# Optimization experiments

Hardware: AMD Instinct MI355X
Metric: run time of the kernel (lower is better)

Reference implementation:

```python
import jax, jax.numpy as jnp
import numpy as np

N = 8192
F_IN = 512
F_HID = 256
ALPHA = 0.2  # LeakyReLU negative slope
NEG_INF = -9e15


def gat_layer(h, adj, W, a):
    """Standard dense GraphAttentionLayer (pyGAT style).
    h: [N, F_in], adj: [N, N] (0/1), W: [F_in, F_out], a: [2*F_out, 1].
    """
    Wh = h @ W  # [N, F_out]
    f_out = W.shape[1]
    # e_ij = leakyrelu(a1 . Wh_i + a2 . Wh_j) via broadcasting
    e1 = Wh @ a[:f_out]      # [N, 1]
    e2 = Wh @ a[f_out:]      # [N, 1]
    e = jax.nn.leaky_relu(e1 + e2.T, negative_slope=ALPHA)  # [N, N]
    e = jnp.where(adj > 0, e, NEG_INF)
    att = jax.nn.softmax(e, axis=-1)  # masked row softmax
    return jax.nn.elu(att @ Wh)       # [N, F_out]


def setup_inputs() -> dict:
    key = jax.random.key(0)
    k_x, k_adj, k_w1, k_a1, k_w2, k_a2 = jax.random.split(key, 6)
    x = jax.random.normal(k_x, (N, F_IN), dtype=jnp.float32)
    # sparse random adjacency (~avg degree 16) + self loops
    adj = (jax.random.uniform(k_adj, (N, N)) < (16.0 / N)).astype(jnp.float32)
    adj = jnp.clip(adj + jnp.eye(N, dtype=jnp.float32), 0.0, 1.0)
    # Xavier-ish init for layer params
    W1 = jax.random.normal(k_w1, (F_IN, F_HID), dtype=jnp.float32) * (1.0 / np.sqrt(F_IN))
    a1 = jax.random.normal(k_a1, (2 * F_HID, 1), dtype=jnp.float32) * (1.0 / np.sqrt(2 * F_HID))
    W2 = jax.random.normal(k_w2, (F_HID, F_IN), dtype=jnp.float32) * (1.0 / np.sqrt(F_HID))
    a2 = jax.random.normal(k_a2, (2 * F_IN, 1), dtype=jnp.float32) * (1.0 / np.sqrt(2 * F_IN))
    return {"x": x, "adj": adj, "W1": W1, "a1": a1, "W2": W2, "a2": a2}


def reference(x, adj, W1, a1, W2, a2):
    enc = gat_layer(x, adj, W1, a1)    # encode: [N, F_HID]
    dec = gat_layer(enc, adj, W2, a2)  # decode: [N, F_IN]
    return (dec, enc)
```

## Files before the change

kernel.cpp:

```cpp
#include <hip/hip_runtime.h>
#include <hip/hip_bf16.h>

#define N_NODES 8192
#define F_IN    512
#define F_HID   256
#define ALPHA   0.2f
#define MAXDEG  64

using f32x4 = __attribute__((ext_vector_type(4))) float;
using f16x8 = __attribute__((ext_vector_type(8))) _Float16;
using f16x4 = __attribute__((ext_vector_type(4))) _Float16;

__global__ void conv_WT(const float* __restrict__ W1, const float* __restrict__ W2,
                        _Float16* __restrict__ W1T, _Float16* __restrict__ W2T,
                        float* __restrict__ stz) {
    int gid = blockIdx.x * blockDim.x + threadIdx.x;
    if (gid < 4 * N_NODES) stz[gid] = 0.0f;

    int t = blockIdx.x;
    const float* W; _Float16* WT; int K, N, kt, nt;
    if (t < 128) { W = W1; WT = W1T; K = 512; N = 256; kt = t & 15; nt = t >> 4; }
    else { t -= 128; W = W2; WT = W2T; K = 256; N = 512; kt = t & 7; nt = t >> 3; }
    __shared__ float Ws[32][33];
    const int tx = threadIdx.x & 31, ty = threadIdx.x >> 5;
    #pragma unroll
    for (int i = 0; i < 4; ++i)
        Ws[ty + 8 * i][tx] = W[(size_t)(kt * 32 + ty + 8 * i) * N + nt * 32 + tx];
    __syncthreads();
    #pragma unroll
    for (int i = 0; i < 4; ++i)
        WT[(size_t)(nt * 32 + ty + 8 * i) * K + kt * 32 + tx] = (_Float16)Ws[tx][ty + 8 * i];
}

__device__ inline void csr_row(const float* __restrict__ adj, int* __restrict__ cols,
                               int* __restrict__ cnt, int row, int lane) {
    const float4* arow = (const float4*)(adj + (size_t)row * N_NODES);
    int* crow = cols + (size_t)row * MAXDEG;
    int count = 0;
    const unsigned long long mlt = (1ULL << lane) - 1ULL;
    for (int base = 0; base < N_NODES; base += 256) {
        float4 v = arow[(base >> 2) + lane];
        unsigned long long b0 = __ballot(v.x > 0.0f);
        unsigned long long b1 = __ballot(v.y > 0.0f);
        unsigned long long b2 = __ballot(v.z > 0.0f);
        unsigned long long b3 = __ballot(v.w > 0.0f);
        int o = count + __popcll(b0 & mlt) + __popcll(b1 & mlt)
                      + __popcll(b2 & mlt) + __popcll(b3 & mlt);
        int c0 = base + (lane << 2);
        if (v.x > 0.0f) { if (o < MAXDEG) crow[o] = c0;     o++; }
        if (v.y > 0.0f) { if (o < MAXDEG) crow[o] = c0 + 1; o++; }
        if (v.z > 0.0f) { if (o < MAXDEG) crow[o] = c0 + 2; o++; }
        if (v.w > 0.0f) { if (o < MAXDEG) crow[o] = c0 + 3; o++; }
        count += __popcll(b0) + __popcll(b1) + __popcll(b2) + __popcll(b3);
    }
    if (lane == 0) cnt[row] = count > MAXDEG ? MAXDEG : count;
}

__device__ inline void gemm1_tile(const float* __restrict__ x,
                                  const _Float16* __restrict__ W1T,
                                  _Float16* __restrict__ Wh1,
                                  const float* __restrict__ a1,
                                  float* __restrict__ s1, float* __restrict__ t1,
                                  int brow, int bcol) {
    const int LDT = 72;
    __shared__ _Float16 As[64 * LDT];
    __shared__ _Float16 Bs[64 * LDT];
    const int tid = threadIdx.x;
    const int wid = tid >> 6, lane = tid & 63;
    const int wr = (wid >> 1) * 32, wc = (wid & 1) * 32;
    const int sr = tid >> 3, skg = (tid & 7) * 8;

    f32x4 acc[2][2];
    #pragma unroll
    for (int m = 0; m < 2; ++m)
        #pragma unroll
        for (int n = 0; n < 2; ++n) acc[m][n] = f32x4{0.f, 0.f, 0.f, 0.f};

    for (int k0 = 0; k0 < F_IN; k0 += 64) {
        #pragma unroll
        for (int i = 0; i < 2; ++i) {
            int r = sr + i * 32;
            const float* src = x + (size_t)(brow + r) * F_IN + k0 + skg;
            f32x4 a0 = *(const f32x4*)src;
            f32x4 a1v = *(const f32x4*)(src + 4);
            f16x8 av;
            #pragma unroll
            for (int j = 0; j < 4; ++j) { av[j] = (_Float16)a0[j]; av[4 + j] = (_Float16)a1v[j]; }
            *(f16x8*)&As[r * LDT + skg] = av;
            *(f16x8*)&Bs[r * LDT + skg] = *(const f16x8*)&W1T[(size_t)(bcol + r) * F_IN + k0 + skg];
        }
        __syncthreads();
        #pragma unroll
        for (int ks = 0; ks < 2; ++ks) {
            const int kb = ks * 32 + (lane >> 4) * 8;
            f16x8 af[2], bfr[2];
            #pragma unroll
            for (int m = 0; m < 2; ++m)
                af[m] = *(const f16x8*)&As[(wr + m * 16 + (lane & 15)) * LDT + kb];
            #pragma unroll
            for (int n = 0; n < 2; ++n)
                bfr[n] = *(const f16x8*)&Bs[(wc + n * 16 + (lane & 15)) * LDT + kb];
            #pragma unroll
            for (int m = 0; m < 2; ++m)
                #pragma unroll
                for (int n = 0; n < 2; ++n)
                    acc[m][n] = __builtin_amdgcn_mfma_f32_16x16x32_f16(
                        af[m], bfr[n], acc[m][n], 0, 0, 0);
        }
        __syncthreads();
    }
    const int c0 = bcol + wc + (lane & 15);
    float as0 = a1[c0],      as1 = a1[c0 + 16];
    float at0 = a1[F_HID + c0], at1 = a1[F_HID + c0 + 16];
    #pragma unroll
    for (int m = 0; m < 2; ++m) {
        #pragma unroll
        for (int j = 0; j < 4; ++j) {
            float vs = acc[m][0][j] * as0 + acc[m][1][j] * as1;
            float vt = acc[m][0][j] * at0 + acc[m][1][j] * at1;
            #pragma unroll
            for (int off = 1; off < 16; off <<= 1) {
                vs += __shfl_xor(vs, off);
                vt += __shfl_xor(vt, off);
            }
            if ((lane & 15) == 0) {
                int row = brow + wr + m * 16 + ((lane >> 4) << 2) + j;
                atomicAdd(s1 + row, vs);
                atomicAdd(t1 + row, vt);
            }
        }
        #pragma unroll
        for (int n = 0; n < 2; ++n) {
            int row = brow + wr + m * 16 + ((lane >> 4) << 2);
            int col = bcol + wc + n * 16 + (lane & 15);
            #pragma unroll
            for (int j = 0; j < 4; ++j)
                Wh1[(size_t)(row + j) * F_HID + col] = (_Float16)acc[m][n][j];
        }
    }
}

__global__ __launch_bounds__(256)
void csr_and_gemm1(const float* __restrict__ adj, int* __restrict__ cols,
                   int* __restrict__ cnt, const float* __restrict__ x,
                   const _Float16* __restrict__ W1T, _Float16* __restrict__ Wh1,
                   const float* __restrict__ a1,
                   float* __restrict__ s1, float* __restrict__ t1) {
    const int bid = blockIdx.x;
    const int g = bid / 5, r = bid % 5;
    if (r == 0) {
        gemm1_tile(x, W1T, Wh1, a1, s1, t1, (g >> 2) * 64, (g & 3) * 64);
    } else {
        const int cb = g * 4 + (r - 1);
        const int row = cb * 4 + (threadIdx.x >> 6);
        csr_row(adj, cols, cnt, row, threadIdx.x & 63);
    }
}

__global__ __launch_bounds__(256)
void gemm2_f16(const _Float16* __restrict__ A, const _Float16* __restrict__ BT,
               _Float16* __restrict__ C, const float* __restrict__ a2,
               float* __restrict__ s2, float* __restrict__ t2) {
    const int LDT = 72;
    __shared__ _Float16 As[128 * LDT];
    __shared__ _Float16 Bs[64 * LDT];
    const int tid = threadIdx.x;
    const int wid = tid >> 6, lane = tid & 63;
    const int brow = (blockIdx.x >> 3) * 128;
    const int bcol = (blockIdx.x & 7) * 64;
    const int wr = (wid >> 1) * 64, wc = (wid & 1) * 32;
    const int sr = tid >> 3, skg = (tid & 7) * 8;

    f32x4 acc[4][2];
    #pragma unroll
    for (int m = 0; m < 4; ++m)
        #pragma unroll
        for (int n = 0; n < 2; ++n) acc[m][n] = f32x4{0.f, 0.f, 0.f, 0.f};

    for (int k0 = 0; k0 < F_HID; k0 += 64) {
        #pragma unroll
        for (int i = 0; i < 4; ++i) {
            int r = sr + i * 32;
            *(f16x8*)&As[r * LDT + skg] = *(const f16x8*)&A[(size_t)(brow + r) * F_HID + k0 + skg];
            if (i < 2)
                *(f16x8*)&Bs[(r & 63) * LDT + skg] =
                    *(const f16x8*)&BT[(size_t)(bcol + (r & 63)) * F_HID + k0 + skg];
        }
        __syncthreads();
        #pragma unroll
        for (int ks = 0; ks < 2; ++ks) {
            const int kb = ks * 32 + (lane >> 4) * 8;
            f16x8 af[4], bfr[2];
            #pragma unroll
            for (int m = 0; m < 4; ++m)
                af[m] = *(const f16x8*)&As[(wr + m * 16 + (lane & 15)) * LDT + kb];
            #pragma unroll
            for (int n = 0; n < 2; ++n)
                bfr[n] = *(const f16x8*)&Bs[(wc + n * 16 + (lane & 15)) * LDT + kb];
            #pragma unroll
            for (int m = 0; m < 4; ++m)
                #pragma unroll
                for (int n = 0; n < 2; ++n)
                    acc[m][n] = __builtin_amdgcn_mfma_f32_16x16x32_f16(
                        af[m], bfr[n], acc[m][n], 0, 0, 0);
        }
        __syncthreads();
    }
    const int c0 = bcol + wc + (lane & 15);
    float as0 = a2[c0],        as1 = a2[c0 + 16];
    float at0 = a2[F_IN + c0], at1 = a2[F_IN + c0 + 16];
    #pragma unroll
    for (int m = 0; m < 4; ++m) {
        #pragma unroll
        for (int j = 0; j < 4; ++j) {
            float vs = acc[m][0][j] * as0 + acc[m][1][j] * as1;
            float vt = acc[m][0][j] * at0 + acc[m][1][j] * at1;
            #pragma unroll
            for (int off = 1; off < 16; off <<= 1) {
                vs += __shfl_xor(vs, off);
                vt += __shfl_xor(vt, off);
            }
            if ((lane & 15) == 0) {
                int row = brow + wr + m * 16 + ((lane >> 4) << 2) + j;
                atomicAdd(s2 + row, vs);
                atomicAdd(t2 + row, vt);
            }
        }
        #pragma unroll
        for (int n = 0; n < 2; ++n) {
            int row = brow + wr + m * 16 + ((lane >> 4) << 2);
            int col = bcol + wc + n * 16 + (lane & 15);
            #pragma unroll
            for (int j = 0; j < 4; ++j)
                C[(size_t)(row + j) * F_IN + col] = (_Float16)acc[m][n][j];
        }
    }
}

template<int F>
__global__ void aggregate16(const _Float16* __restrict__ Wh,
                            const int* __restrict__ cols, const int* __restrict__ cnt,
                            const float* __restrict__ s, const float* __restrict__ t,
                            float* __restrict__ out, _Float16* __restrict__ out16) {
    const int EL = F / 64;
    const int wid = threadIdx.x >> 6, lane = threadIdx.x & 63;
    const int row = blockIdx.x * 4 + wid;
    const int deg = cnt[row];
    __shared__ float pS[4][64];
    __shared__ int jS[4][64];
    int j = 0;
    float ev = -1e30f;
    if (lane < deg) {
        j = cols[(size_t)row * MAXDEG + lane];
        float z = s[row] + t[j];
        ev = z > 0.0f ? z : ALPHA * z;
    }
    float m = ev;
    #pragma unroll
    for (int off = 32; off > 0; off >>= 1) m = fmaxf(m, __shfl_xor(m, off));
    float ex = (lane < deg) ? __expf(ev - m) : 0.0f;
    float sum = ex;
    #pragma unroll
    for (int off = 32; off > 0; off >>= 1) sum += __shfl_xor(sum, off);
    pS[wid][lane] = ex / sum;
    jS[wid][lane] = j;
    __syncthreads();

    float acc[EL] = {};
    const size_t lo = (size_t)lane * EL;
    int d = 0;
    for (; d + 4 <= deg; d += 4) {
        float p0 = pS[wid][d],     p1 = pS[wid][d + 1];
        float p2 = pS[wid][d + 2], p3 = pS[wid][d + 3];
        const _Float16* w0 = Wh + (size_t)jS[wid][d] * F + lo;
        const _Float16* w1 = Wh + (size_t)jS[wid][d + 1] * F + lo;
        const _Float16* w2 = Wh + (size_t)jS[wid][d + 2] * F + lo;
        const _Float16* w3 = Wh + (size_t)jS[wid][d + 3] * F + lo;
        if constexpr (EL == 8) {
            f16x8 v0 = *(const f16x8*)w0, v1 = *(const f16x8*)w1;
            f16x8 v2 = *(const f16x8*)w2, v3 = *(const f16x8*)w3;
            #pragma unroll
            for (int jj = 0; jj < 8; ++jj)
                acc[jj] += p0 * (float)v0[jj] + p1 * (float)v1[jj]
                         + p2 * (float)v2[jj] + p3 * (float)v3[jj];
        } else {
            f16x4 v0 = *(const f16x4*)w0, v1 = *(const f16x4*)w1;
            f16x4 v2 = *(const f16x4*)w2, v3 = *(const f16x4*)w3;
            #pragma unroll
            for (int jj = 0; jj < 4; ++jj)
                acc[jj] += p0 * (float)v0[jj] + p1 * (float)v1[jj]
                         + p2 * (float)v2[jj] + p3 * (float)v3[jj];
        }
    }
    for (; d < deg; ++d) {
        float p = pS[wid][d];
        const _Float16* wr = Wh + (size_t)jS[wid][d] * F + lo;
        if constexpr (EL == 8) {
            f16x8 w = *(const f16x8*)wr;
            #pragma unroll
            for (int jj = 0; jj < 8; ++jj) acc[jj] += p * (float)w[jj];
        } else {
            f16x4 w = *(const f16x4*)wr;
            #pragma unroll
            for (int jj = 0; jj < 4; ++jj) acc[jj] += p * (float)w[jj];
        }
    }
    #pragma unroll
    for (int c = 0; c < EL / 4; ++c) {
        f32x4 o; f16x4 h;
        #pragma unroll
        for (int jj = 0; jj < 4; ++jj) {
            float v = acc[c * 4 + jj];
            float e = v > 0.0f ? v : (__expf(v) - 1.0f);
            o[jj] = e; h[jj] = (_Float16)e;
        }
        *(f32x4*)(out + (size_t)row * F + lo + c * 4) = o;
        if (out16)
            *(f16x4*)(out16 + (size_t)row * F + lo + c * 4) = h;
    }
}

extern "C" void kernel_launch(void* const* d_in, const int* in_sizes, int n_in,
                              void* d_out, int out_size, void* d_ws, size_t ws_size,
                              hipStream_t stream) {
    (void)in_sizes; (void)n_in; (void)out_size; (void)ws_size;
    const float* x   = (const float*)d_in[0];
    const float* adj = (const float*)d_in[1];
    const float* W1  = (const float*)d_in[2];
    const float* a1  = (const float*)d_in[3];
    const float* W2  = (const float*)d_in[4];
    const float* a2  = (const float*)d_in[5];

    float* dec = (float*)d_out;
    float* enc = dec + (size_t)N_NODES * F_IN;

    int*      cols  = (int*)d_ws;
    int*      cnt   = cols + (size_t)N_NODES * MAXDEG;
    float*    s1    = (float*)(cnt + N_NODES);
    float*    t1    = s1 + N_NODES;
    float*    s2    = t1 + N_NODES;
    float*    t2    = s2 + N_NODES;
    _Float16* Wh1   = (_Float16*)(t2 + N_NODES);
    _Float16* Wh2   = Wh1 + (size_t)N_NODES * F_HID;
    _Float16* enc16 = Wh2 + (size_t)N_NODES * F_IN;
    _Float16* W1T   = enc16 + (size_t)N_NODES * F_HID;
    _Float16* W2T   = W1T + (size_t)F_HID * F_IN;

    conv_WT<<<256, 256, 0, stream>>>(W1, W2, W1T, W2T, s1);

    csr_and_gemm1<<<2560, 256, 0, stream>>>(adj, cols, cnt, x, W1T, Wh1, a1, s1, t1);

    aggregate16<F_HID><<<N_NODES / 4, 256, 0, stream>>>(Wh1, cols, cnt, s1, t1, enc, enc16);

    gemm2_f16<<<512, 256, 0, stream>>>(enc16, W2T, Wh2, a2, s2, t2);

    aggregate16<F_IN><<<N_NODES / 4, 256, 0, stream>>>(Wh2, cols, cnt, s2, t2, dec, (_Float16*)nullptr);
}
```

Baseline: 113.1 us.

## Use nontemporal loads/stores, widen CSR scan, stage full B in gemm2, unroll aggregation by 8

The adjacency scan now processes 512 columns per iteration with two nontemporal vector loads, and the x loads in gemm1 are also nontemporal. gemm2 loads its whole 64x256 B tile into shared memory once instead of once per k-step, which removes repeated B traffic at the cost of more LDS. The attention aggregation gains an 8-neighbor unrolled loop that puts more gathers in flight. Output stores use nontemporal hints. More LDS and registers may lower occupancy.

```diff
diff --git a/kernel.cpp b/kernel.cpp
--- a/kernel.cpp
+++ b/kernel.cpp
@@ -34,24 +34,37 @@
 
 __device__ inline void csr_row(const float* __restrict__ adj, int* __restrict__ cols,
                                int* __restrict__ cnt, int row, int lane) {
-    const float4* arow = (const float4*)(adj + (size_t)row * N_NODES);
+    const f32x4* arow = (const f32x4*)(adj + (size_t)row * N_NODES);
     int* crow = cols + (size_t)row * MAXDEG;
     int count = 0;
     const unsigned long long mlt = (1ULL << lane) - 1ULL;
-    for (int base = 0; base < N_NODES; base += 256) {
-        float4 v = arow[(base >> 2) + lane];
-        unsigned long long b0 = __ballot(v.x > 0.0f);
-        unsigned long long b1 = __ballot(v.y > 0.0f);
-        unsigned long long b2 = __ballot(v.z > 0.0f);
-        unsigned long long b3 = __ballot(v.w > 0.0f);
+    for (int base = 0; base < N_NODES; base += 512) {
+        f32x4 v0 = __builtin_nontemporal_load(&arow[(base >> 2) + lane]);
+        f32x4 v1 = __builtin_nontemporal_load(&arow[(base >> 2) + 64 + lane]);
+        unsigned long long b0 = __ballot(v0[0] > 0.0f);
+        unsigned long long b1 = __ballot(v0[1] > 0.0f);
+        unsigned long long b2 = __ballot(v0[2] > 0.0f);
+        unsigned long long b3 = __ballot(v0[3] > 0.0f);
+        unsigned long long b4 = __ballot(v1[0] > 0.0f);
+        unsigned long long b5 = __ballot(v1[1] > 0.0f);
+        unsigned long long b6 = __ballot(v1[2] > 0.0f);
+        unsigned long long b7 = __ballot(v1[3] > 0.0f);
         int o = count + __popcll(b0 & mlt) + __popcll(b1 & mlt)
                       + __popcll(b2 & mlt) + __popcll(b3 & mlt);
         int c0 = base + (lane << 2);
-        if (v.x > 0.0f) { if (o < MAXDEG) crow[o] = c0;     o++; }
-        if (v.y > 0.0f) { if (o < MAXDEG) crow[o] = c0 + 1; o++; }
-        if (v.z > 0.0f) { if (o < MAXDEG) crow[o] = c0 + 2; o++; }
-        if (v.w > 0.0f) { if (o < MAXDEG) crow[o] = c0 + 3; o++; }
+        if (v0[0] > 0.0f) { if (o < MAXDEG) crow[o] = c0;     o++; }
+        if (v0[1] > 0.0f) { if (o < MAXDEG) crow[o] = c0 + 1; o++; }
+        if (v0[2] > 0.0f) { if (o < MAXDEG) crow[o] = c0 + 2; o++; }
+        if (v0[3] > 0.0f) { if (o < MAXDEG) crow[o] = c0 + 3; o++; }
         count += __popcll(b0) + __popcll(b1) + __popcll(b2) + __popcll(b3);
+        o = count + __popcll(b4 & mlt) + __popcll(b5 & mlt)
+                  + __popcll(b6 & mlt) + __popcll(b7 & mlt);
+        int c1 = base + 256 + (lane << 2);
+        if (v1[0] > 0.0f) { if (o < MAXDEG) crow[o] = c1;     o++; }
+        if (v1[1] > 0.0f) { if (o < MAXDEG) crow[o] = c1 + 1; o++; }
+        if (v1[2] > 0.0f) { if (o < MAXDEG) crow[o] = c1 + 2; o++; }
+        if (v1[3] > 0.0f) { if (o < MAXDEG) crow[o] = c1 + 3; o++; }
+        count += __popcll(b4) + __popcll(b5) + __popcll(b6) + __popcll(b7);
     }
     if (lane == 0) cnt[row] = count > MAXDEG ? MAXDEG : count;
 }
@@ -80,9 +93,9 @@
         #pragma unroll
         for (int i = 0; i < 2; ++i) {
             int r = sr + i * 32;
-            const float* src = x + (size_t)(brow + r) * F_IN + k0 + skg;
-            f32x4 a0 = *(const f32x4*)src;
-            f32x4 a1v = *(const f32x4*)(src + 4);
+            const f32x4* src = (const f32x4*)(x + (size_t)(brow + r) * F_IN + k0 + skg);
+            f32x4 a0 = __builtin_nontemporal_load(src);
+            f32x4 a1v = __builtin_nontemporal_load(src + 1);
             f16x8 av;
             #pragma unroll
             for (int j = 0; j < 4; ++j) { av[j] = (_Float16)a0[j]; av[4 + j] = (_Float16)a1v[j]; }
@@ -110,7 +123,7 @@
         __syncthreads();
     }
     const int c0 = bcol + wc + (lane & 15);
-    float as0 = a1[c0],      as1 = a1[c0 + 16];
+    float as0 = a1[c0],         as1 = a1[c0 + 16];
     float at0 = a1[F_HID + c0], at1 = a1[F_HID + c0 + 16];
     #pragma unroll
     for (int m = 0; m < 2; ++m) {
@@ -161,15 +174,21 @@
 void gemm2_f16(const _Float16* __restrict__ A, const _Float16* __restrict__ BT,
                _Float16* __restrict__ C, const float* __restrict__ a2,
                float* __restrict__ s2, float* __restrict__ t2) {
-    const int LDT = 72;
+    const int LDT = 72, LDB = 264;
     __shared__ _Float16 As[128 * LDT];
-    __shared__ _Float16 Bs[64 * LDT];
+    __shared__ _Float16 Bs[64 * LDB];
     const int tid = threadIdx.x;
     const int wid = tid >> 6, lane = tid & 63;
     const int brow = (blockIdx.x >> 3) * 128;
     const int bcol = (blockIdx.x & 7) * 64;
     const int wr = (wid >> 1) * 64, wc = (wid & 1) * 32;
-    const int sr = tid >> 3, skg = (tid & 7) * 8;
+
+    #pragma unroll
+    for (int i = 0; i < 8; ++i) {
+        int id = tid + i * 256;
+        int r = id >> 5, kc = (id & 31) * 8;
+        *(f16x8*)&Bs[r * LDB + kc] = *(const f16x8*)&BT[(size_t)(bcol + r) * F_HID + kc];
+    }
 
     f32x4 acc[4][2];
     #pragma unroll
@@ -180,11 +199,9 @@
     for (int k0 = 0; k0 < F_HID; k0 += 64) {
         #pragma unroll
         for (int i = 0; i < 4; ++i) {
-            int r = sr + i * 32;
-            *(f16x8*)&As[r * LDT + skg] = *(const f16x8*)&A[(size_t)(brow + r) * F_HID + k0 + skg];
-            if (i < 2)
-                *(f16x8*)&Bs[(r & 63) * LDT + skg] =
-                    *(const f16x8*)&BT[(size_t)(bcol + (r & 63)) * F_HID + k0 + skg];
+            int id = tid + i * 256;
+            int r = id >> 3, kc = (id & 7) * 8;
+            *(f16x8*)&As[r * LDT + kc] = *(const f16x8*)&A[(size_t)(brow + r) * F_HID + k0 + kc];
         }
         __syncthreads();
         #pragma unroll
@@ -196,7 +213,7 @@
                 af[m] = *(const f16x8*)&As[(wr + m * 16 + (lane & 15)) * LDT + kb];
             #pragma unroll
             for (int n = 0; n < 2; ++n)
-                bfr[n] = *(const f16x8*)&Bs[(wc + n * 16 + (lane & 15)) * LDT + kb];
+                bfr[n] = *(const f16x8*)&Bs[(wc + n * 16 + (lane & 15)) * LDB + k0 + kb];
             #pragma unroll
             for (int m = 0; m < 4; ++m)
                 #pragma unroll
@@ -269,6 +286,37 @@
     float acc[EL] = {};
     const size_t lo = (size_t)lane * EL;
     int d = 0;
+    for (; d + 8 <= deg; d += 8) {
+        float p[8]; const _Float16* w[8];
+        #pragma unroll
+        for (int q = 0; q < 8; ++q) {
+            p[q] = pS[wid][d + q];
+            w[q] = Wh + (size_t)jS[wid][d + q] * F + lo;
+        }
+        if constexpr (EL == 8) {
+            f16x8 v[8];
+            #pragma unroll
+            for (int q = 0; q < 8; ++q) v[q] = *(const f16x8*)w[q];
+            #pragma unroll
+            for (int jj = 0; jj < 8; ++jj) {
+                float a = 0.f;
+                #pragma unroll
+                for (int q = 0; q < 8; ++q) a += p[q] * (float)v[q][jj];
+                acc[jj] += a;
+            }
+        } else {
+            f16x4 v[8];
+            #pragma unroll
+            for (int q = 0; q < 8; ++q) v[q] = *(const f16x4*)w[q];
+            #pragma unroll
+            for (int jj = 0; jj < 4; ++jj) {
+                float a = 0.f;
+                #pragma unroll
+                for (int q = 0; q < 8; ++q) a += p[q] * (float)v[q][jj];
+                acc[jj] += a;
+            }
+        }
+    }
     for (; d + 4 <= deg; d += 4) {
         float p0 = pS[wid][d],     p1 = pS[wid][d + 1];
         float p2 = pS[wid][d + 2], p3 = pS[wid][d + 3];
@@ -314,7 +362,7 @@
             float e = v > 0.0f ? v : (__expf(v) - 1.0f);
             o[jj] = e; h[jj] = (_Float16)e;
         }
-        *(f32x4*)(out + (size_t)row * F + lo + c * 4) = o;
+        __builtin_nontemporal_store(o, (f32x4*)(out + (size_t)row * F + lo + c * 4));
         if (out16)
             *(f16x4*)(out16 + (size_t)row * F + lo + c * 4) = h;
     }
```

Measured after the change: 114.4 us. About the same (+1.2%).
